# Optimization experiments

Hardware: AMD Instinct MI355X
Metric: run time of the kernel (lower is better)

Reference implementation:

```python
import jax, jax.numpy as jnp
import numpy as np

N_NODES = 50000
IN_CH = 256
Z_DIM = 64
N_EDGES = 800000


def setup_inputs() -> dict:
    key = jax.random.key(0)
    k_x, k_e, k_wm, k_ws = jax.random.split(key, 4)
    x = jax.random.normal(k_x, (N_NODES, IN_CH), dtype=jnp.float32)
    edge_index = jax.random.randint(k_e, (2, N_EDGES), 0, N_NODES, dtype=jnp.int64)
    # Glorot-style init like PyG GCNConv
    scale = 1.0 / np.sqrt(IN_CH)
    W_mu = jax.random.uniform(k_wm, (IN_CH, Z_DIM), dtype=jnp.float32, minval=-scale, maxval=scale)
    W_logstd = jax.random.uniform(k_ws, (IN_CH, Z_DIM), dtype=jnp.float32, minval=-scale, maxval=scale)
    b_mu = jnp.zeros((Z_DIM,), dtype=jnp.float32)
    b_logstd = jnp.zeros((Z_DIM,), dtype=jnp.float32)
    return {"x": x, "edge_index": edge_index, "W_mu": W_mu, "b_mu": b_mu,
            "W_logstd": W_logstd, "b_logstd": b_logstd}


def _gcn_conv(x, W, b, src, dst, deg_inv_sqrt, num_nodes):
    # PyG GCNConv: out = D^{-1/2} (A + I) D^{-1/2} X W + b
    xw = x @ W                                   # [N, Z]
    norm = deg_inv_sqrt[src] * deg_inv_sqrt[dst]  # [E+N]
    msg = xw[src] * norm[:, None]                 # gather + scale, [E+N, Z]
    agg = jax.ops.segment_sum(msg, dst, num_segments=num_nodes)  # scatter-add
    return agg + b


def reference(x, edge_index, W_mu, b_mu, W_logstd, b_logstd):
    num_nodes = x.shape[0]
    loops = jnp.arange(num_nodes, dtype=edge_index.dtype)
    src = jnp.concatenate([edge_index[0], loops])
    dst = jnp.concatenate([edge_index[1], loops])
    # degree (with self loops) on target nodes, symmetric normalization
    deg = jax.ops.segment_sum(jnp.ones_like(dst, dtype=x.dtype), dst, num_segments=num_nodes)
    deg_inv_sqrt = jnp.where(deg > 0, jax.lax.rsqrt(jnp.maximum(deg, 1.0)), 0.0)
    mu = _gcn_conv(x, W_mu, b_mu, src, dst, deg_inv_sqrt, num_nodes)
    logstd = _gcn_conv(x, W_logstd, b_logstd, src, dst, deg_inv_sqrt, num_nodes)
    return (mu, logstd)
```

## Files before the change

kernel.cpp:

```cpp
#include <hip/hip_runtime.h>

#define N_NODES 50000
#define IN_CH   256
#define Z_DIM   64
#define N_EDGES 800000
#define CH2     128
#define NODE_OFF (N_NODES * Z_DIM)
#define NBLK    ((N_NODES + 255) / 256)
#define SEG     8
#define NBUCKET (SEG * N_NODES)
#define CAP     16
#define EBLKS   (N_EDGES / 256)
#define NW      32768
#define WBLKS   (NW / 256)

typedef __bf16 bf16x8 __attribute__((ext_vector_type(8)));
typedef float  f32x4  __attribute__((ext_vector_type(4)));

__device__ __forceinline__ unsigned short f2bf(float f) {
    unsigned u = __float_as_uint(f);
    return (unsigned short)((u + 0x7FFF + ((u >> 16) & 1)) >> 16);
}
__device__ __forceinline__ float bf_lo(unsigned w) { return __uint_as_float(w << 16); }
__device__ __forceinline__ float bf_hi(unsigned w) { return __uint_as_float(w & 0xFFFF0000u); }

__global__ void k_scatter_w(const int* __restrict__ src, const int* __restrict__ dst,
                            const float* __restrict__ Wmu, const float* __restrict__ Wls,
                            int* __restrict__ cur8, unsigned short* __restrict__ pk2,
                            unsigned short* __restrict__ WbT) {
    int b = blockIdx.x;
    if (b < EBLKS) {
        int e = b * 256 + threadIdx.x;
        int s = src[e];
        int d = dst[e];
        int seg = b & (SEG - 1);
        int idx = seg * N_NODES + d;
        int pos = atomicAdd(&cur8[idx], 1);
        if (pos < CAP) pk2[(size_t)idx * CAP + pos] = (unsigned short)s;
    } else {
        int g = (b - EBLKS) * 256 + threadIdx.x;
        int n = g >> 8, k = g & 255;
        float v = (n < 64) ? Wmu[(size_t)k * 64 + n] : Wls[(size_t)k * 64 + (n - 64)];
        WbT[(size_t)n * 256 + k] = f2bf(v);
    }
}

__global__ void k_dinv(const int* __restrict__ cur8, float* __restrict__ dinv) {
    int i = blockIdx.x * 256 + threadIdx.x;
    if (i >= N_NODES) return;
    int t = 1;
#pragma unroll
    for (int x = 0; x < SEG; ++x) t += cur8[x * N_NODES + i];
    dinv[i] = rsqrtf((float)t);
}

#define LDP 264
#define CSP 132
__global__ __launch_bounds__(256) void k_gemm(const float* __restrict__ x,
                                              const unsigned short* __restrict__ WbT,
                                              unsigned short* __restrict__ xwb) {
    __shared__ __align__(16) char smem[32 * LDP * 2];
    unsigned short* As = (unsigned short*)smem;
    float*          Cs = (float*)smem;
    const int tid = threadIdx.x;
    const int r0  = blockIdx.x * 32;

    {
        int row_l = tid >> 3;
        int cb    = (tid & 7) * 32;
        int row   = r0 + row_l;
        unsigned short* dp = As + row_l * LDP + cb;
        if (row < N_NODES) {
            const float4* xp = (const float4*)(x + (size_t)row * IN_CH + cb);
#pragma unroll
            for (int i = 0; i < 4; ++i) {
                float4 a = xp[2 * i];
                float4 b = xp[2 * i + 1];
                uint4 w;
                w.x = (unsigned)f2bf(a.x) | ((unsigned)f2bf(a.y) << 16);
                w.y = (unsigned)f2bf(a.z) | ((unsigned)f2bf(a.w) << 16);
                w.z = (unsigned)f2bf(b.x) | ((unsigned)f2bf(b.y) << 16);
                w.w = (unsigned)f2bf(b.z) | ((unsigned)f2bf(b.w) << 16);
                *(uint4*)(dp + i * 8) = w;
            }
        } else {
            uint4 z = make_uint4(0, 0, 0, 0);
#pragma unroll
            for (int i = 0; i < 4; ++i) *(uint4*)(dp + i * 8) = z;
        }
    }
    __syncthreads();

    const int wv   = tid >> 6;
    const int lane = tid & 63;
    const int m    = lane & 15;
    const int q    = lane >> 4;
    const int row_half = (wv & 1) * 16;
    const int col_half = (wv >> 1) * 64;

    f32x4 acc[4] = {};
    const unsigned short* ap = As + (row_half + m) * LDP + q * 8;
    const unsigned short* bp = WbT + (size_t)(col_half + m) * 256 + q * 8;

#pragma unroll
    for (int k0 = 0; k0 < IN_CH; k0 += 32) {
        bf16x8 af = *(const bf16x8*)(ap + k0);
#pragma unroll
        for (int nt = 0; nt < 4; ++nt) {
            bf16x8 bf_ = *(const bf16x8*)(bp + (size_t)nt * 16 * 256 + k0);
            acc[nt] = __builtin_amdgcn_mfma_f32_16x16x32_bf16(af, bf_, acc[nt], 0, 0, 0);
        }
    }

    __syncthreads();
#pragma unroll
    for (int nt = 0; nt < 4; ++nt)
#pragma unroll
        for (int r = 0; r < 4; ++r)
            Cs[(row_half + q * 4 + r) * CSP + col_half + nt * 16 + m] = acc[nt][r];
    __syncthreads();

    {
        int row_l = tid >> 3;
        int c0    = (tid & 7) * 16;
        int row   = r0 + row_l;
        if (row < N_NODES) {
            const float* cp = Cs + row_l * CSP + c0;
            float4 a = *(const float4*)(cp + 0);
            float4 b = *(const float4*)(cp + 4);
            float4 c = *(const float4*)(cp + 8);
            float4 d = *(const float4*)(cp + 12);
            uint4 w0, w1;
            w0.x = (unsigned)f2bf(a.x) | ((unsigned)f2bf(a.y) << 16);
            w0.y = (unsigned)f2bf(a.z) | ((unsigned)f2bf(a.w) << 16);
            w0.z = (unsigned)f2bf(b.x) | ((unsigned)f2bf(b.y) << 16);
            w0.w = (unsigned)f2bf(b.z) | ((unsigned)f2bf(b.w) << 16);
            w1.x = (unsigned)f2bf(c.x) | ((unsigned)f2bf(c.y) << 16);
            w1.y = (unsigned)f2bf(c.z) | ((unsigned)f2bf(c.w) << 16);
            w1.z = (unsigned)f2bf(d.x) | ((unsigned)f2bf(d.y) << 16);
            w1.w = (unsigned)f2bf(d.z) | ((unsigned)f2bf(d.w) << 16);
            uint4* op = (uint4*)(xwb + (size_t)row * CH2 + c0);
            op[0] = w0;
            op[1] = w1;
        }
    }
}

__global__ __launch_bounds__(256) void k_gather(const int* __restrict__ cur8,
                                                const unsigned short* __restrict__ pk2,
                                                const unsigned short* __restrict__ xwb,
                                                const float* __restrict__ dinv,
                                                const float* __restrict__ bmu,
                                                const float* __restrict__ bls,
                                                float* __restrict__ out) {
    const int i    = blockIdx.x * 4 + (threadIdx.x >> 6);
    const int lane = threadIdx.x & 63;
    const int q    = lane >> 4;
    const int cl   = lane & 15;

    float di = dinv[i];
    float acc[8] = {0.f, 0.f, 0.f, 0.f, 0.f, 0.f, 0.f, 0.f};
    if (q == 0) {
        float sq = di * di;
        uint4 w = *(const uint4*)(xwb + (size_t)i * CH2 + cl * 8);
        acc[0] = bf_lo(w.x) * sq; acc[1] = bf_hi(w.x) * sq;
        acc[2] = bf_lo(w.y) * sq; acc[3] = bf_hi(w.y) * sq;
        acc[4] = bf_lo(w.z) * sq; acc[5] = bf_hi(w.z) * sq;
        acc[6] = bf_lo(w.w) * sq; acc[7] = bf_hi(w.w) * sq;
    }

#pragma unroll
    for (int b = 0; b < 2; ++b) {
        int idx = (q + b * 4) * N_NODES + i;
        int cnt = cur8[idx];
        if (cnt > CAP) cnt = CAP;
        size_t base = (size_t)idx * CAP;
        for (int j = 0; j < cnt; ++j) {
            int s = pk2[base + j];
            float nrm = di * dinv[s];
            uint4 w = *(const uint4*)(xwb + (size_t)s * CH2 + cl * 8);
            acc[0] += bf_lo(w.x) * nrm; acc[1] += bf_hi(w.x) * nrm;
            acc[2] += bf_lo(w.y) * nrm; acc[3] += bf_hi(w.y) * nrm;
            acc[4] += bf_lo(w.z) * nrm; acc[5] += bf_hi(w.z) * nrm;
            acc[6] += bf_lo(w.w) * nrm; acc[7] += bf_hi(w.w) * nrm;
        }
    }

#pragma unroll
    for (int k = 0; k < 8; ++k) {
        acc[k] += __shfl_xor(acc[k], 16);
        acc[k] += __shfl_xor(acc[k], 32);
    }

    if (lane < 16) {
        int c0 = cl * 8;
        const float* bb = (c0 < 64) ? (bmu + c0) : (bls + (c0 - 64));
        float4 b0 = *(const float4*)(bb + 0);
        float4 b1 = *(const float4*)(bb + 4);
        float* o = (c0 < 64) ? (out + (size_t)i * 64 + c0)
                             : (out + NODE_OFF + (size_t)i * 64 + (c0 - 64));
        *(float4*)(o + 0) = make_float4(acc[0] + b0.x, acc[1] + b0.y, acc[2] + b0.z, acc[3] + b0.w);
        *(float4*)(o + 4) = make_float4(acc[4] + b1.x, acc[5] + b1.y, acc[6] + b1.z, acc[7] + b1.w);
    }
}

extern "C" void kernel_launch(void* const* d_in, const int* in_sizes, int n_in,
                              void* d_out, int out_size, void* d_ws, size_t ws_size,
                              hipStream_t stream) {
    const float* x   = (const float*)d_in[0];
    const int*   ei  = (const int*)d_in[1];
    const float* Wmu = (const float*)d_in[2];
    const float* bmu = (const float*)d_in[3];
    const float* Wls = (const float*)d_in[4];
    const float* bls = (const float*)d_in[5];
    float* out = (float*)d_out;

    const int* src = ei;
    const int* dst = ei + N_EDGES;

    char* ws = (char*)d_ws;
    int*            cur8 = (int*)(ws + 0);
    float*          dinv = (float*)(ws + 1638400);
    unsigned short* WbT  = (unsigned short*)(ws + 1867776);
    unsigned short* pk2  = (unsigned short*)(ws + 2097152);
    unsigned short* xwb  = (unsigned short*)(ws + 16777216);

    hipMemsetAsync(cur8, 0, NBUCKET * sizeof(int), stream);
    k_scatter_w<<<EBLKS + WBLKS, 256, 0, stream>>>(src, dst, Wmu, Wls, cur8, pk2, WbT);
    k_gemm<<<(N_NODES + 31) / 32, 256, 0, stream>>>(x, WbT, xwb);
    k_dinv<<<NBLK, 256, 0, stream>>>(cur8, dinv);
    k_gather<<<N_NODES / 4, 256, 0, stream>>>(cur8, pk2, xwb, dinv, bmu, bls, out);
}
```

Before: 229.1 us.

## Fuse all stages into one persistent kernel with grid barriers

Replaces the memset plus four separate launches with one persistent kernel of fixed grid size that runs the stages separated by software grid barriers. It also splits blocks so the GEMM tiles and the edge scatter run concurrently in the same phase. The goal is to remove launch gaps and let the two independent stages overlap. The cost is spin-wait barrier overhead, and correctness depends on all 768 blocks being co-resident. Gather parallelism is also limited to a grid-stride loop.

```diff
diff --git a/kernel.cpp b/kernel.cpp
--- a/kernel.cpp
+++ b/kernel.cpp
@@ -6,13 +6,17 @@
 #define N_EDGES 800000
 #define CH2     128
 #define NODE_OFF (N_NODES * Z_DIM)
-#define NBLK    ((N_NODES + 255) / 256)
 #define SEG     8
 #define NBUCKET (SEG * N_NODES)
 #define CAP     16
-#define EBLKS   (N_EDGES / 256)
+#define ECHUNKS (N_EDGES / 256)
 #define NW      32768
-#define WBLKS   (NW / 256)
+
+#define GRID    768
+#define GEMM_B  320
+#define SCAT_B  448
+#define NTILES  ((N_NODES + 31) / 32)
+#define NGRP    (N_NODES / 4)
 
 typedef __bf16 bf16x8 __attribute__((ext_vector_type(8)));
 typedef float  f32x4  __attribute__((ext_vector_type(4)));
@@ -24,46 +28,28 @@
 __device__ __forceinline__ float bf_lo(unsigned w) { return __uint_as_float(w << 16); }
 __device__ __forceinline__ float bf_hi(unsigned w) { return __uint_as_float(w & 0xFFFF0000u); }
 
-__global__ void k_scatter_w(const int* __restrict__ src, const int* __restrict__ dst,
-                            const float* __restrict__ Wmu, const float* __restrict__ Wls,
-                            int* __restrict__ cur8, unsigned short* __restrict__ pk2,
-                            unsigned short* __restrict__ WbT) {
-    int b = blockIdx.x;
-    if (b < EBLKS) {
-        int e = b * 256 + threadIdx.x;
-        int s = src[e];
-        int d = dst[e];
-        int seg = b & (SEG - 1);
-        int idx = seg * N_NODES + d;
-        int pos = atomicAdd(&cur8[idx], 1);
-        if (pos < CAP) pk2[(size_t)idx * CAP + pos] = (unsigned short)s;
-    } else {
-        int g = (b - EBLKS) * 256 + threadIdx.x;
-        int n = g >> 8, k = g & 255;
-        float v = (n < 64) ? Wmu[(size_t)k * 64 + n] : Wls[(size_t)k * 64 + (n - 64)];
-        WbT[(size_t)n * 256 + k] = f2bf(v);
-    }
-}
-
-__global__ void k_dinv(const int* __restrict__ cur8, float* __restrict__ dinv) {
-    int i = blockIdx.x * 256 + threadIdx.x;
-    if (i >= N_NODES) return;
-    int t = 1;
-#pragma unroll
-    for (int x = 0; x < SEG; ++x) t += cur8[x * N_NODES + i];
-    dinv[i] = rsqrtf((float)t);
+__device__ __forceinline__ void gbar(int* cnt) {
+    __syncthreads();
+    if (threadIdx.x == 0) {
+        __threadfence();
+        atomicAdd(cnt, 1);
+        while (__hip_atomic_load(cnt, __ATOMIC_RELAXED, __HIP_MEMORY_SCOPE_AGENT) < GRID)
+            __builtin_amdgcn_s_sleep(2);
+        __threadfence();
+    }
+    __syncthreads();
 }
 
 #define LDP 264
 #define CSP 132
-__global__ __launch_bounds__(256) void k_gemm(const float* __restrict__ x,
-                                              const unsigned short* __restrict__ WbT,
-                                              unsigned short* __restrict__ xwb) {
-    __shared__ __align__(16) char smem[32 * LDP * 2];
+
+__device__ void gemm_tile(int t, const float* __restrict__ x,
+                          const unsigned short* __restrict__ WbT,
+                          unsigned short* __restrict__ xwb, char* smem) {
     unsigned short* As = (unsigned short*)smem;
     float*          Cs = (float*)smem;
     const int tid = threadIdx.x;
-    const int r0  = blockIdx.x * 32;
+    const int r0  = t * 32;
 
     {
         int row_l = tid >> 3;
@@ -144,63 +130,111 @@
             op[1] = w1;
         }
     }
-}
-
-__global__ __launch_bounds__(256) void k_gather(const int* __restrict__ cur8,
-                                                const unsigned short* __restrict__ pk2,
-                                                const unsigned short* __restrict__ xwb,
-                                                const float* __restrict__ dinv,
-                                                const float* __restrict__ bmu,
-                                                const float* __restrict__ bls,
-                                                float* __restrict__ out) {
-    const int i    = blockIdx.x * 4 + (threadIdx.x >> 6);
-    const int lane = threadIdx.x & 63;
+    __syncthreads();
+}
+
+__global__ __launch_bounds__(256, 4) void k_mega(
+    const float* __restrict__ x, const int* __restrict__ src, const int* __restrict__ dst,
+    const float* __restrict__ Wmu, const float* __restrict__ bmu,
+    const float* __restrict__ Wls, const float* __restrict__ bls,
+    int* __restrict__ cur8, float* __restrict__ dinv,
+    unsigned short* __restrict__ WbT, unsigned short* __restrict__ pk2,
+    unsigned short* __restrict__ xwb, int* __restrict__ bars,
+    float* __restrict__ out) {
+    __shared__ __align__(16) char smem[32 * LDP * 2];
+    const int tid = threadIdx.x;
+
+    for (int idx = blockIdx.x * 256 + tid; idx < NBUCKET + NW; idx += GRID * 256) {
+        if (idx < NBUCKET) {
+            cur8[idx] = 0;
+        } else {
+            int h = idx - NBUCKET;
+            int n = h >> 8, k = h & 255;
+            float v = (n < 64) ? Wmu[(size_t)k * 64 + n] : Wls[(size_t)k * 64 + (n - 64)];
+            WbT[(size_t)n * 256 + k] = f2bf(v);
+        }
+    }
+    gbar(bars + 0);
+
+    if (blockIdx.x < GEMM_B) {
+        for (int t = blockIdx.x; t < NTILES; t += GEMM_B)
+            gemm_tile(t, x, WbT, xwb, smem);
+    } else {
+        for (int c = blockIdx.x - GEMM_B; c < ECHUNKS; c += SCAT_B) {
+            int e = c * 256 + tid;
+            int s = src[e];
+            int d = dst[e];
+            int seg = c & (SEG - 1);
+            int idx = seg * N_NODES + d;
+            int pos = atomicAdd(&cur8[idx], 1);
+            if (pos < CAP) pk2[(size_t)idx * CAP + pos] = (unsigned short)s;
+        }
+    }
+    gbar(bars + 1);
+
+    {
+        int i = blockIdx.x * 256 + tid;
+        if (i < N_NODES) {
+            int t = 1;
+#pragma unroll
+            for (int xg = 0; xg < SEG; ++xg) t += cur8[xg * N_NODES + i];
+            dinv[i] = rsqrtf((float)t);
+        }
+    }
+    gbar(bars + 2);
+
+    const int lane = tid & 63;
     const int q    = lane >> 4;
     const int cl   = lane & 15;
-
-    float di = dinv[i];
-    float acc[8] = {0.f, 0.f, 0.f, 0.f, 0.f, 0.f, 0.f, 0.f};
-    if (q == 0) {
-        float sq = di * di;
-        uint4 w = *(const uint4*)(xwb + (size_t)i * CH2 + cl * 8);
-        acc[0] = bf_lo(w.x) * sq; acc[1] = bf_hi(w.x) * sq;
-        acc[2] = bf_lo(w.y) * sq; acc[3] = bf_hi(w.y) * sq;
-        acc[4] = bf_lo(w.z) * sq; acc[5] = bf_hi(w.z) * sq;
-        acc[6] = bf_lo(w.w) * sq; acc[7] = bf_hi(w.w) * sq;
-    }
-
-#pragma unroll
-    for (int b = 0; b < 2; ++b) {
-        int idx = (q + b * 4) * N_NODES + i;
-        int cnt = cur8[idx];
-        if (cnt > CAP) cnt = CAP;
-        size_t base = (size_t)idx * CAP;
-        for (int j = 0; j < cnt; ++j) {
-            int s = pk2[base + j];
-            float nrm = di * dinv[s];
-            uint4 w = *(const uint4*)(xwb + (size_t)s * CH2 + cl * 8);
-            acc[0] += bf_lo(w.x) * nrm; acc[1] += bf_hi(w.x) * nrm;
-            acc[2] += bf_lo(w.y) * nrm; acc[3] += bf_hi(w.y) * nrm;
-            acc[4] += bf_lo(w.z) * nrm; acc[5] += bf_hi(w.z) * nrm;
-            acc[6] += bf_lo(w.w) * nrm; acc[7] += bf_hi(w.w) * nrm;
-        }
-    }
-
-#pragma unroll
-    for (int k = 0; k < 8; ++k) {
-        acc[k] += __shfl_xor(acc[k], 16);
-        acc[k] += __shfl_xor(acc[k], 32);
-    }
-
-    if (lane < 16) {
-        int c0 = cl * 8;
-        const float* bb = (c0 < 64) ? (bmu + c0) : (bls + (c0 - 64));
-        float4 b0 = *(const float4*)(bb + 0);
-        float4 b1 = *(const float4*)(bb + 4);
-        float* o = (c0 < 64) ? (out + (size_t)i * 64 + c0)
-                             : (out + NODE_OFF + (size_t)i * 64 + (c0 - 64));
-        *(float4*)(o + 0) = make_float4(acc[0] + b0.x, acc[1] + b0.y, acc[2] + b0.z, acc[3] + b0.w);
-        *(float4*)(o + 4) = make_float4(acc[4] + b1.x, acc[5] + b1.y, acc[6] + b1.z, acc[7] + b1.w);
+    for (int g = blockIdx.x; g < NGRP; g += GRID) {
+        const int i = g * 4 + (tid >> 6);
+
+        float di = dinv[i];
+        float acc[8] = {0.f, 0.f, 0.f, 0.f, 0.f, 0.f, 0.f, 0.f};
+        if (q == 0) {
+            float sq = di * di;
+            uint4 w = *(const uint4*)(xwb + (size_t)i * CH2 + cl * 8);
+            acc[0] = bf_lo(w.x) * sq; acc[1] = bf_hi(w.x) * sq;
+            acc[2] = bf_lo(w.y) * sq; acc[3] = bf_hi(w.y) * sq;
+            acc[4] = bf_lo(w.z) * sq; acc[5] = bf_hi(w.z) * sq;
+            acc[6] = bf_lo(w.w) * sq; acc[7] = bf_hi(w.w) * sq;
+        }
+
+#pragma unroll
+        for (int b = 0; b < 2; ++b) {
+            int idx = (q + b * 4) * N_NODES + i;
+            int cnt = cur8[idx];
+            if (cnt > CAP) cnt = CAP;
+            size_t base = (size_t)idx * CAP;
+            for (int j = 0; j < cnt; ++j) {
+                int s = pk2[base + j];
+                float nrm = di * dinv[s];
+                uint4 w = *(const uint4*)(xwb + (size_t)s * CH2 + cl * 8);
+                acc[0] += bf_lo(w.x) * nrm; acc[1] += bf_hi(w.x) * nrm;
+                acc[2] += bf_lo(w.y) * nrm; acc[3] += bf_hi(w.y) * nrm;
+                acc[4] += bf_lo(w.z) * nrm; acc[5] += bf_hi(w.z) * nrm;
+                acc[6] += bf_lo(w.w) * nrm; acc[7] += bf_hi(w.w) * nrm;
+            }
+        }
+
+#pragma unroll
+        for (int k = 0; k < 8; ++k) {
+            acc[k] += __shfl_xor(acc[k], 16);
+            acc[k] += __shfl_xor(acc[k], 32);
+        }
+
+        if (lane < 16) {
+            int c0 = cl * 8;
+            const float* bb = (c0 < 64) ? (bmu + c0) : (bls + (c0 - 64));
+            float4 b0 = *(const float4*)(bb + 0);
+            float4 b1 = *(const float4*)(bb + 4);
+            float* o = (c0 < 64) ? (out + (size_t)i * 64 + c0)
+                                 : (out + NODE_OFF + (size_t)i * 64 + (c0 - 64));
+            *(float4*)(o + 0) = make_float4(acc[0] + b0.x, acc[1] + b0.y,
+                                            acc[2] + b0.z, acc[3] + b0.w);
+            *(float4*)(o + 4) = make_float4(acc[4] + b1.x, acc[5] + b1.y,
+                                            acc[6] + b1.z, acc[7] + b1.w);
+        }
     }
 }
 
@@ -222,12 +256,11 @@
     int*            cur8 = (int*)(ws + 0);
     float*          dinv = (float*)(ws + 1638400);
     unsigned short* WbT  = (unsigned short*)(ws + 1867776);
+    int*            bars = (int*)(ws + 1998848);
     unsigned short* pk2  = (unsigned short*)(ws + 2097152);
     unsigned short* xwb  = (unsigned short*)(ws + 16777216);
 
-    hipMemsetAsync(cur8, 0, NBUCKET * sizeof(int), stream);
-    k_scatter_w<<<EBLKS + WBLKS, 256, 0, stream>>>(src, dst, Wmu, Wls, cur8, pk2, WbT);
-    k_gemm<<<(N_NODES + 31) / 32, 256, 0, stream>>>(x, WbT, xwb);
-    k_dinv<<<NBLK, 256, 0, stream>>>(cur8, dinv);
-    k_gather<<<N_NODES / 4, 256, 0, stream>>>(cur8, pk2, xwb, dinv, bmu, bls, out);
-}
+    hipMemsetAsync(bars, 0, 3 * sizeof(int), stream);
+    k_mega<<<GRID, 256, 0, stream>>>(x, src, dst, Wmu, bmu, Wls, bls,
+                                     cur8, dinv, WbT, pk2, xwb, bars, out);
+}
```

Result: slower. 521.9 us (+127.8%).

## Fuse memset into prep kernel and co-schedule GEMM with edge scatter

Applied to the files above, without the earlier changes.

Replaces the hipMemsetAsync with a prep kernel that zeroes the bucket counters and transposes and converts the weights to bf16. The GEMM tiles and the edge-scatter blocks now share one launch, so the bandwidth-bound x read can overlap with the atomic scatter. The GEMM epilogue converts to bf16 before writing to shared memory, which halves LDS traffic, and it uses the compiler's native bf16 conversion. This cuts one launch and the idle gaps between stages. The cost is a larger kernel, since scatter blocks reserve the GEMM's shared memory, which may lower occupancy.

```diff
diff --git a/kernel.cpp b/kernel.cpp
--- a/kernel.cpp
+++ b/kernel.cpp
@@ -10,60 +10,44 @@
 #define SEG     8
 #define NBUCKET (SEG * N_NODES)
 #define CAP     16
-#define EBLKS   (N_EDGES / 256)
+#define ECHUNKS (N_EDGES / 256)
+#define NTILES  ((N_NODES + 31) / 32)
 #define NW      32768
-#define WBLKS   (NW / 256)
 
 typedef __bf16 bf16x8 __attribute__((ext_vector_type(8)));
 typedef float  f32x4  __attribute__((ext_vector_type(4)));
 
 __device__ __forceinline__ unsigned short f2bf(float f) {
-    unsigned u = __float_as_uint(f);
-    return (unsigned short)((u + 0x7FFF + ((u >> 16) & 1)) >> 16);
+    __bf16 h = (__bf16)f;
+    unsigned short u;
+    __builtin_memcpy(&u, &h, 2);
+    return u;
 }
 __device__ __forceinline__ float bf_lo(unsigned w) { return __uint_as_float(w << 16); }
 __device__ __forceinline__ float bf_hi(unsigned w) { return __uint_as_float(w & 0xFFFF0000u); }
 
-__global__ void k_scatter_w(const int* __restrict__ src, const int* __restrict__ dst,
-                            const float* __restrict__ Wmu, const float* __restrict__ Wls,
-                            int* __restrict__ cur8, unsigned short* __restrict__ pk2,
-                            unsigned short* __restrict__ WbT) {
-    int b = blockIdx.x;
-    if (b < EBLKS) {
-        int e = b * 256 + threadIdx.x;
-        int s = src[e];
-        int d = dst[e];
-        int seg = b & (SEG - 1);
-        int idx = seg * N_NODES + d;
-        int pos = atomicAdd(&cur8[idx], 1);
-        if (pos < CAP) pk2[(size_t)idx * CAP + pos] = (unsigned short)s;
-    } else {
-        int g = (b - EBLKS) * 256 + threadIdx.x;
-        int n = g >> 8, k = g & 255;
+__global__ void k_pre(int* __restrict__ cur8,
+                      const float* __restrict__ Wmu, const float* __restrict__ Wls,
+                      unsigned short* __restrict__ WbT) {
+    int g = blockIdx.x * 256 + threadIdx.x;
+    if (g < NBUCKET) cur8[g] = 0;
+    int h = g - NBUCKET;
+    if (h >= 0 && h < NW) {
+        int n = h >> 8, k = h & 255;
         float v = (n < 64) ? Wmu[(size_t)k * 64 + n] : Wls[(size_t)k * 64 + (n - 64)];
         WbT[(size_t)n * 256 + k] = f2bf(v);
     }
 }
 
-__global__ void k_dinv(const int* __restrict__ cur8, float* __restrict__ dinv) {
-    int i = blockIdx.x * 256 + threadIdx.x;
-    if (i >= N_NODES) return;
-    int t = 1;
-#pragma unroll
-    for (int x = 0; x < SEG; ++x) t += cur8[x * N_NODES + i];
-    dinv[i] = rsqrtf((float)t);
-}
-
-#define LDP 264
-#define CSP 132
-__global__ __launch_bounds__(256) void k_gemm(const float* __restrict__ x,
-                                              const unsigned short* __restrict__ WbT,
-                                              unsigned short* __restrict__ xwb) {
-    __shared__ __align__(16) char smem[32 * LDP * 2];
-    unsigned short* As = (unsigned short*)smem;
-    float*          Cs = (float*)smem;
+#define LDP  264
+#define CSP2 136
+__device__ __forceinline__ void gemm_tile(int t, const float* __restrict__ x,
+                                          const unsigned short* __restrict__ WbT,
+                                          unsigned short* __restrict__ xwb, char* smem) {
+    unsigned short* As  = (unsigned short*)smem;
+    unsigned short* Css = (unsigned short*)smem;
     const int tid = threadIdx.x;
-    const int r0  = blockIdx.x * 32;
+    const int r0  = t * 32;
 
     {
         int row_l = tid >> 3;
@@ -117,7 +101,7 @@
     for (int nt = 0; nt < 4; ++nt)
 #pragma unroll
         for (int r = 0; r < 4; ++r)
-            Cs[(row_half + q * 4 + r) * CSP + col_half + nt * 16 + m] = acc[nt][r];
+            Css[(row_half + q * 4 + r) * CSP2 + col_half + nt * 16 + m] = f2bf(acc[nt][r]);
     __syncthreads();
 
     {
@@ -125,25 +109,44 @@
         int c0    = (tid & 7) * 16;
         int row   = r0 + row_l;
         if (row < N_NODES) {
-            const float* cp = Cs + row_l * CSP + c0;
-            float4 a = *(const float4*)(cp + 0);
-            float4 b = *(const float4*)(cp + 4);
-            float4 c = *(const float4*)(cp + 8);
-            float4 d = *(const float4*)(cp + 12);
-            uint4 w0, w1;
-            w0.x = (unsigned)f2bf(a.x) | ((unsigned)f2bf(a.y) << 16);
-            w0.y = (unsigned)f2bf(a.z) | ((unsigned)f2bf(a.w) << 16);
-            w0.z = (unsigned)f2bf(b.x) | ((unsigned)f2bf(b.y) << 16);
-            w0.w = (unsigned)f2bf(b.z) | ((unsigned)f2bf(b.w) << 16);
-            w1.x = (unsigned)f2bf(c.x) | ((unsigned)f2bf(c.y) << 16);
-            w1.y = (unsigned)f2bf(c.z) | ((unsigned)f2bf(c.w) << 16);
-            w1.z = (unsigned)f2bf(d.x) | ((unsigned)f2bf(d.y) << 16);
-            w1.w = (unsigned)f2bf(d.z) | ((unsigned)f2bf(d.w) << 16);
+            const uint4* cp = (const uint4*)(Css + row_l * CSP2 + c0);
+            uint4 w0 = cp[0];
+            uint4 w1 = cp[1];
             uint4* op = (uint4*)(xwb + (size_t)row * CH2 + c0);
             op[0] = w0;
             op[1] = w1;
         }
     }
+    __syncthreads();
+}
+
+__global__ __launch_bounds__(256) void k_gemm_scat(
+    const float* __restrict__ x, const unsigned short* __restrict__ WbT,
+    unsigned short* __restrict__ xwb,
+    const int* __restrict__ src, const int* __restrict__ dst,
+    int* __restrict__ cur8, unsigned short* __restrict__ pk2) {
+    __shared__ __align__(16) char smem[32 * LDP * 2];
+    if (blockIdx.x < NTILES) {
+        gemm_tile(blockIdx.x, x, WbT, xwb, smem);
+    } else {
+        int c = blockIdx.x - NTILES;
+        int e = c * 256 + threadIdx.x;
+        int s = src[e];
+        int d = dst[e];
+        int seg = c & (SEG - 1);
+        int idx = seg * N_NODES + d;
+        int pos = atomicAdd(&cur8[idx], 1);
+        if (pos < CAP) pk2[(size_t)idx * CAP + pos] = (unsigned short)s;
+    }
+}
+
+__global__ void k_dinv(const int* __restrict__ cur8, float* __restrict__ dinv) {
+    int i = blockIdx.x * 256 + threadIdx.x;
+    if (i >= N_NODES) return;
+    int t = 1;
+#pragma unroll
+    for (int xg = 0; xg < SEG; ++xg) t += cur8[xg * N_NODES + i];
+    dinv[i] = rsqrtf((float)t);
 }
 
 __global__ __launch_bounds__(256) void k_gather(const int* __restrict__ cur8,
@@ -199,8 +202,10 @@
         float4 b1 = *(const float4*)(bb + 4);
         float* o = (c0 < 64) ? (out + (size_t)i * 64 + c0)
                              : (out + NODE_OFF + (size_t)i * 64 + (c0 - 64));
-        *(float4*)(o + 0) = make_float4(acc[0] + b0.x, acc[1] + b0.y, acc[2] + b0.z, acc[3] + b0.w);
-        *(float4*)(o + 4) = make_float4(acc[4] + b1.x, acc[5] + b1.y, acc[6] + b1.z, acc[7] + b1.w);
+        *(float4*)(o + 0) = make_float4(acc[0] + b0.x, acc[1] + b0.y,
+                                        acc[2] + b0.z, acc[3] + b0.w);
+        *(float4*)(o + 4) = make_float4(acc[4] + b1.x, acc[5] + b1.y,
+                                        acc[6] + b1.z, acc[7] + b1.w);
     }
 }
 
@@ -225,9 +230,8 @@
     unsigned short* pk2  = (unsigned short*)(ws + 2097152);
     unsigned short* xwb  = (unsigned short*)(ws + 16777216);
 
-    hipMemsetAsync(cur8, 0, NBUCKET * sizeof(int), stream);
-    k_scatter_w<<<EBLKS + WBLKS, 256, 0, stream>>>(src, dst, Wmu, Wls, cur8, pk2, WbT);
-    k_gemm<<<(N_NODES + 31) / 32, 256, 0, stream>>>(x, WbT, xwb);
+    k_pre<<<(NBUCKET + NW + 255) / 256, 256, 0, stream>>>(cur8, Wmu, Wls, WbT);
+    k_gemm_scat<<<NTILES + ECHUNKS, 256, 0, stream>>>(x, WbT, xwb, src, dst, cur8, pk2);
     k_dinv<<<NBLK, 256, 0, stream>>>(cur8, dinv);
     k_gather<<<N_NODES / 4, 256, 0, stream>>>(cur8, pk2, xwb, dinv, bmu, bls, out);
 }
```

Measured after the change: 226.0 us. No clear change (-1.4%).
